# Kernel optimization log

Measured on AMD Instinct MI355X. Metric: run time of the kernel, lower is better.

## Reference

```python
import jax, jax.numpy as jnp
import numpy as np

NL, NK = 10000, 2000          # ligand / keypoint node counts
ELL, EKL = 320000, 160000     # lig->lig and kp->lig edge counts
IN, HID, OUT = 128, 128, 128  # in_size, hidden_size, out_size
FDIM = 2 * IN + 1             # edge MLP input: [h_src, h_dst, dij]


def silu(x):
    return x * jax.nn.sigmoid(x)


def setup_inputs() -> dict:
    keys = iter(jax.random.split(jax.random.key(0), 64))

    def nrm(shape, scale=0.02):
        return jax.random.normal(next(keys), shape, dtype=jnp.float32) * scale

    d = {}
    d["h_lig"] = jax.random.normal(next(keys), (NL, IN), dtype=jnp.float32)
    d["h_kp"] = jax.random.normal(next(keys), (NK, IN), dtype=jnp.float32)
    d["x_lig"] = jax.random.normal(next(keys), (NL, 3), dtype=jnp.float32)
    d["x_kp"] = jax.random.normal(next(keys), (NK, 3), dtype=jnp.float32)
    # per-node normalizer (e.g. neighbor count); keep >= 1 to avoid blowup
    d["z_lig"] = jax.random.uniform(next(keys), (NL, 1), dtype=jnp.float32, minval=1.0, maxval=32.0)
    for e in ("ll", "kl"):
        d[e + "_eW1"] = nrm((FDIM, HID)); d[e + "_eb1"] = jnp.zeros((HID,), jnp.float32)
        d[e + "_eW2"] = nrm((HID, HID)); d[e + "_eb2"] = jnp.zeros((HID,), jnp.float32)
        d[e + "_aW"] = nrm((HID, 1)); d[e + "_ab"] = jnp.zeros((1,), jnp.float32)
        d[e + "_cW1"] = nrm((FDIM, HID)); d[e + "_cb1"] = jnp.zeros((HID,), jnp.float32)
        d[e + "_cW2"] = nrm((HID, HID)); d[e + "_cb2"] = jnp.zeros((HID,), jnp.float32)
        d[e + "_cW3"] = nrm((HID, 1), scale=0.001)  # xavier gain=0.001 final coord layer
    d["n_W1"] = nrm((IN + HID, HID)); d["n_b1"] = jnp.zeros((HID,), jnp.float32)
    d["n_W2"] = nrm((HID, OUT)); d["n_b2"] = jnp.zeros((OUT,), jnp.float32)
    d["ll_src"] = jax.random.randint(next(keys), (ELL,), 0, NL, dtype=jnp.int32)
    d["ll_dst"] = jax.random.randint(next(keys), (ELL,), 0, NL, dtype=jnp.int32)
    d["kl_src"] = jax.random.randint(next(keys), (EKL,), 0, NK, dtype=jnp.int32)
    d["kl_dst"] = jax.random.randint(next(keys), (EKL,), 0, NL, dtype=jnp.int32)
    return d


def _edge_messages(hs, hd, xs, xd, eW1, eb1, eW2, eb2, aW, ab, cW1, cb1, cW2, cb2, cW3):
    x_diff = xs - xd                                     # fn.u_sub_v
    dij = jnp.linalg.norm(x_diff, axis=1, keepdims=True)  # [E,1]
    x_diff = x_diff / (dij + 1.0)
    f = jnp.concatenate([hs, hd, dij], axis=1)           # [E, 2*IN+1]
    m = silu(f @ eW1 + eb1)
    m = silu(m @ eW2 + eb2)
    msg_h = m * jax.nn.sigmoid(m @ aW + ab)              # soft attention gate
    c = silu(f @ cW1 + cb1)
    c = silu(c @ cW2 + cb2)
    msg_x = (c @ cW3) * x_diff                           # use_tanh=False path
    return msg_h, msg_x


def reference(h_lig, h_kp, x_lig, x_kp, z_lig,
              ll_eW1, ll_eb1, ll_eW2, ll_eb2, ll_aW, ll_ab,
              ll_cW1, ll_cb1, ll_cW2, ll_cb2, ll_cW3,
              kl_eW1, kl_eb1, kl_eW2, kl_eb2, kl_aW, kl_ab,
              kl_cW1, kl_cb1, kl_cW2, kl_cb2, kl_cW3,
              n_W1, n_b1, n_W2, n_b2,
              ll_src, ll_dst, kl_src, kl_dst):
    # lig -> lig edges
    mh_ll, mx_ll = _edge_messages(h_lig[ll_src], h_lig[ll_dst], x_lig[ll_src], x_lig[ll_dst],
                                  ll_eW1, ll_eb1, ll_eW2, ll_eb2, ll_aW, ll_ab,
                                  ll_cW1, ll_cb1, ll_cW2, ll_cb2, ll_cW3)
    # kp -> lig edges
    mh_kl, mx_kl = _edge_messages(h_kp[kl_src], h_lig[kl_dst], x_kp[kl_src], x_lig[kl_dst],
                                  kl_eW1, kl_eb1, kl_eW2, kl_eb2, kl_aW, kl_ab,
                                  kl_cW1, kl_cb1, kl_cW2, kl_cb2, kl_cW3)
    nl = h_lig.shape[0]
    # multi_update_all with cross_reducer='sum', then per-node normalization by z
    h_neigh = (jax.ops.segment_sum(mh_ll, ll_dst, num_segments=nl)
               + jax.ops.segment_sum(mh_kl, kl_dst, num_segments=nl)) / z_lig
    x_neigh = (jax.ops.segment_sum(mx_ll, ll_dst, num_segments=nl)
               + jax.ops.segment_sum(mx_kl, kl_dst, num_segments=nl)) / z_lig
    nin = jnp.concatenate([h_lig, h_neigh], axis=1)
    h_out = h_lig + (silu(nin @ n_W1 + n_b1) @ n_W2 + n_b2)  # norm=False -> Identity
    x_out = x_lig + x_neigh
    return (h_out, x_out)
```

## Files before the change

kernel.cpp:

```cpp
#include <hip/hip_runtime.h>
#include <math.h>

#define EPB  64
#define MSTR 136

typedef __attribute__((ext_vector_type(8))) short short8;
typedef __attribute__((ext_vector_type(4))) float f32x4;

__device__ __forceinline__ unsigned short f2bf(float x) {
    unsigned int u = __float_as_uint(x);
    u += 0x7fffu + ((u >> 16) & 1u);
    return (unsigned short)(u >> 16);
}
__device__ __forceinline__ float bf2f(short v) {
    return __uint_as_float(((unsigned int)(unsigned short)v) << 16);
}
__device__ __forceinline__ float fsilu(float x) {
    return x * (1.0f / (1.0f + __expf(-x)));
}
__device__ __forceinline__ float fsigm(float x) {
    return 1.0f / (1.0f + __expf(-x));
}
__device__ __forceinline__ void atomAddF(float* p, float v) {
    unsafeAtomicAdd(p, v);
}

struct PrepArgs { const float* src[10]; };

__global__ __launch_bounds__(256) void setup_kernel(PrepArgs pa, short* __restrict__ wsb,
                                                    float* __restrict__ out, int out_n,
                                                    int* __restrict__ hist) {
    int idx = blockIdx.x * 256 + threadIdx.x;
    if (idx < 245760) {
        int pair = idx / 49152;
        int rem  = idx - pair * 49152;
        int second = (rem >= 32768) ? 1 : 0;
        int mi = pair * 2 + second;
        int within = second ? (rem - 32768) : rem;
        int n, k, K;
        if (second) { K = 128; n = within >> 7; k = within & 127; }
        else        { K = 256; n = within >> 8; k = within & 255; }
        int dstoff = pair * 49152 + second * 32768;
        wsb[dstoff + n * K + k] = (short)f2bf(pa.src[mi][k * 128 + n]);
        return;
    }
    idx -= 245760;
    if (idx < out_n) { out[idx] = 0.0f; return; }
    idx -= out_n;
    if (idx < 20000) hist[idx] = 0;
}

__global__ __launch_bounds__(256) void hist_kernel(const int* __restrict__ lld,
                                                   const int* __restrict__ kld,
                                                   int* __restrict__ hist) {
    int i = blockIdx.x * 256 + threadIdx.x;
    if (i < 320000) atomicAdd(&hist[lld[i]], 1);
    else if (i < 480000) atomicAdd(&hist[10000 + kld[i - 320000]], 1);
}

__global__ __launch_bounds__(256) void scan_kernel(const int* __restrict__ hist,
                                                   int* __restrict__ cursor) {
    __shared__ int sbuf[256];
    const int b = blockIdx.x, t = threadIdx.x;
    const int* h = hist + b * 10000;
    int* cur = cursor + b * 10000;
    const int base = t * 40;
    int s = 0;
#pragma unroll 8
    for (int i = 0; i < 40; i++) if (base + i < 10000) s += h[base + i];
    sbuf[t] = s;
    __syncthreads();
    for (int off = 1; off < 256; off <<= 1) {
        int v = (t >= off) ? sbuf[t - off] : 0;
        __syncthreads();
        sbuf[t] += v;
        __syncthreads();
    }
    int run = sbuf[t] - s;
    for (int i = 0; i < 40; i++) {
        if (base + i < 10000) { cur[base + i] = run; run += h[base + i]; }
    }
}

__global__ __launch_bounds__(256) void scatter_kernel(const int* __restrict__ lls,
                                                      const int* __restrict__ lld,
                                                      const int* __restrict__ kls,
                                                      const int* __restrict__ kld,
                                                      int* __restrict__ cursor,
                                                      int* __restrict__ ll_ssrc, int* __restrict__ ll_sdst,
                                                      int* __restrict__ kl_ssrc, int* __restrict__ kl_sdst) {
    int i = blockIdx.x * 256 + threadIdx.x;
    if (i < 320000) {
        int d = lld[i];
        int p = atomicAdd(&cursor[d], 1);
        ll_ssrc[p] = lls[i]; ll_sdst[p] = d;
    } else if (i < 480000) {
        int j = i - 320000;
        int d = kld[j];
        int p = atomicAdd(&cursor[10000 + d], 1);
        kl_ssrc[p] = kls[j]; kl_sdst[p] = d;
    }
}

struct ProjDesc { const float* A; const short* Bt; short* out; const float* bias;
                  int rows; int ktb; int co; int hasb; };
struct ProjArgs { ProjDesc d[8]; };

__global__ __launch_bounds__(256) void proj_kernel(ProjArgs pa) {
    const ProjDesc pd = pa.d[blockIdx.y];
    const int tile = blockIdx.x;
    if (tile * 64 >= pd.rows) return;
    __shared__ __align__(16) short a_lds[64 * MSTR];
    const int t = threadIdx.x;
    {
        const int r = t >> 2, q = t & 3;
        const int node = tile * 64 + r;
        short* arow = a_lds + r * MSTR + q * 32;
        if (node < pd.rows) {
            const float* ap = pd.A + (size_t)node * 128 + q * 32;
#pragma unroll
            for (int i = 0; i < 4; i++) {
                float4 v0 = *(const float4*)(ap + i * 8);
                float4 v1 = *(const float4*)(ap + i * 8 + 4);
                short8 o;
                o[0] = (short)f2bf(v0.x); o[1] = (short)f2bf(v0.y);
                o[2] = (short)f2bf(v0.z); o[3] = (short)f2bf(v0.w);
                o[4] = (short)f2bf(v1.x); o[5] = (short)f2bf(v1.y);
                o[6] = (short)f2bf(v1.z); o[7] = (short)f2bf(v1.w);
                *(short8*)(arow + i * 8) = o;
            }
        } else {
            short8 z = {0, 0, 0, 0, 0, 0, 0, 0};
#pragma unroll
            for (int i = 0; i < 4; i++) *(short8*)(arow + i * 8) = z;
        }
    }
    __syncthreads();

    const int ln = t & 63, wv = t >> 6;
    const int lrow = ln & 15, quad = ln >> 4;
    const int c0 = wv * 32 + lrow, c1 = c0 + 16;

    short8 bf0[4], bf1[4];
#pragma unroll
    for (int kt = 0; kt < 4; kt++) {
        bf0[kt] = *(const short8*)(pd.Bt + c0 * 256 + (pd.ktb + kt) * 32 + quad * 8);
        bf1[kt] = *(const short8*)(pd.Bt + c1 * 256 + (pd.ktb + kt) * 32 + quad * 8);
    }
    const float bb0 = pd.hasb ? pd.bias[c0] : 0.0f;
    const float bb1 = pd.hasb ? pd.bias[c1] : 0.0f;
#pragma unroll
    for (int mt = 0; mt < 4; mt++) {
        short8 af[4];
#pragma unroll
        for (int kt = 0; kt < 4; kt++)
            af[kt] = *(const short8*)(&a_lds[(mt * 16 + lrow) * MSTR + kt * 32 + quad * 8]);
        f32x4 a0 = {0.f, 0.f, 0.f, 0.f}, a1 = {0.f, 0.f, 0.f, 0.f};
#pragma unroll
        for (int kt = 0; kt < 4; kt++) {
            a0 = __builtin_amdgcn_mfma_f32_16x16x32_bf16(af[kt], bf0[kt], a0, 0, 0, 0);
            a1 = __builtin_amdgcn_mfma_f32_16x16x32_bf16(af[kt], bf1[kt], a1, 0, 0, 0);
        }
#pragma unroll
        for (int r = 0; r < 4; r++) {
            const int node = tile * 64 + mt * 16 + quad * 4 + r;
            if (node < pd.rows) {
                pd.out[(size_t)node * 256 + pd.co + c0] = (short)f2bf(a0[r] + bb0);
                pd.out[(size_t)node * 256 + pd.co + c1] = (short)f2bf(a1[r] + bb1);
            }
        }
    }
}

struct EdgeSet {
    const short *Ps, *Pd;
    const float *xs, *xd;
    const int *esrc, *edst;
    const float *w256e, *w256c;
    const short *W2t, *cW2t;
    const float *b2e, *b2c;
    const float *aW, *ab, *cW3;
};
struct EdgePair { EdgeSet s[2]; int split; };

__global__ __launch_bounds__(256, 4) void edge_kernel(EdgePair ep,
                                                      float* __restrict__ hne,
                                                      float* __restrict__ xne)
{
    __shared__ __align__(16) char mbuf[34816];
    __shared__ float sv_l[EPB];
    __shared__ float gate_l[EPB];
    __shared__ float xdf[3][EPB];
    __shared__ int   dstl[EPB];
    __shared__ float gp[4][EPB];

    short* mh = (short*)mbuf;
    short* mc = (short*)(mbuf + 17408);
    float* msg = (float*)mbuf;

    const int isKL = (blockIdx.x >= ep.split) ? 1 : 0;
    const EdgeSet P = ep.s[isKL];
    const int bid = blockIdx.x - (isKL ? ep.split : 0);
    const int eb = bid * EPB;
    const int t = threadIdx.x;

    {
        const int e = t >> 2, q = t & 3;
        const int eid = eb + e;
        const int s = P.esrc[eid], d = P.edst[eid];
        float dx = P.xs[s * 3 + 0] - P.xd[d * 3 + 0];
        float dy = P.xs[s * 3 + 1] - P.xd[d * 3 + 1];
        float dz = P.xs[s * 3 + 2] - P.xd[d * 3 + 2];
        float dd = sqrtf(dx * dx + dy * dy + dz * dz);
        if (q == 0) {
            dstl[e] = d;
            float inv = 1.0f / (dd + 1.0f);
            xdf[0][e] = dx * inv; xdf[1][e] = dy * inv; xdf[2][e] = dz * inv;
        }
        const short* psrow = P.Ps + (size_t)s * 256 + q * 32;
        const short* pdrow = P.Pd + (size_t)d * 256 + q * 32;
#pragma unroll
        for (int path = 0; path < 2; path++) {
            const short* ps = psrow + path * 128;
            const short* pq = pdrow + path * 128;
            const float* wq = (path ? P.w256c : P.w256e) + q * 32;
            short* mrow = (path ? mc : mh) + e * MSTR + q * 32;
#pragma unroll
            for (int i = 0; i < 4; i++) {
                short8 a = *(const short8*)(ps + i * 8);
                short8 b = *(const short8*)(pq + i * 8);
                float4 wA = *(const float4*)(wq + i * 8);
                float4 wB = *(const float4*)(wq + i * 8 + 4);
                short8 o;
                o[0] = (short)f2bf(fsilu(bf2f(a[0]) + bf2f(b[0]) + dd * wA.x));
                o[1] = (short)f2bf(fsilu(bf2f(a[1]) + bf2f(b[1]) + dd * wA.y));
                o[2] = (short)f2bf(fsilu(bf2f(a[2]) + bf2f(b[2]) + dd * wA.z));
                o[3] = (short)f2bf(fsilu(bf2f(a[3]) + bf2f(b[3]) + dd * wA.w));
                o[4] = (short)f2bf(fsilu(bf2f(a[4]) + bf2f(b[4]) + dd * wB.x));
                o[5] = (short)f2bf(fsilu(bf2f(a[5]) + bf2f(b[5]) + dd * wB.y));
                o[6] = (short)f2bf(fsilu(bf2f(a[6]) + bf2f(b[6]) + dd * wB.z));
                o[7] = (short)f2bf(fsilu(bf2f(a[7]) + bf2f(b[7]) + dd * wB.w));
                *(short8*)(mrow + i * 8) = o;
            }
        }
    }
    __syncthreads();

    const int ln = t & 63, wv = t >> 6;
    const int lrow = ln & 15, quad = ln >> 4;
    const int c0 = wv * 32 + lrow, c1 = c0 + 16;

    {
        short8 bf0[4], bf1[4];
#pragma unroll
        for (int kt = 0; kt < 4; kt++) {
            bf0[kt] = *(const short8*)(P.cW2t + c0 * 128 + kt * 32 + quad * 8);
            bf1[kt] = *(const short8*)(P.cW2t + c1 * 128 + kt * 32 + quad * 8);
        }
        const float cw0 = P.cW3[c0], cw1 = P.cW3[c1];
        const float bb0 = P.b2c[c0], bb1 = P.b2c[c1];
#pragma unroll
        for (int mt = 0; mt < 4; mt++) {
            short8 af[4];
#pragma unroll
            for (int kt = 0; kt < 4; kt++)
                af[kt] = *(const short8*)(&mc[(mt * 16 + lrow) * MSTR + kt * 32 + quad * 8]);
            f32x4 a0 = {0.f, 0.f, 0.f, 0.f}, a1 = {0.f, 0.f, 0.f, 0.f};
#pragma unroll
            for (int kt = 0; kt < 4; kt++) {
                a0 = __builtin_amdgcn_mfma_f32_16x16x32_bf16(af[kt], bf0[kt], a0, 0, 0, 0);
                a1 = __builtin_amdgcn_mfma_f32_16x16x32_bf16(af[kt], bf1[kt], a1, 0, 0, 0);
            }
#pragma unroll
            for (int r = 0; r < 4; r++) {
                float v0 = fsilu(a0[r] + bb0);
                float v1 = fsilu(a1[r] + bb1);
                float g = v0 * cw0 + v1 * cw1;
                g += __shfl_xor(g, 1, 64);
                g += __shfl_xor(g, 2, 64);
                g += __shfl_xor(g, 4, 64);
                g += __shfl_xor(g, 8, 64);
                if (lrow == 0) gp[wv][mt * 16 + quad * 4 + r] = g;
            }
        }
    }
    __syncthreads();
    if (t < EPB) sv_l[t] = gp[0][t] + gp[1][t] + gp[2][t] + gp[3][t];
    __syncthreads();

    float m2s[4][8];
    {
        short8 bf0[4], bf1[4];
#pragma unroll
        for (int kt = 0; kt < 4; kt++) {
            bf0[kt] = *(const short8*)(P.W2t + c0 * 128 + kt * 32 + quad * 8);
            bf1[kt] = *(const short8*)(P.W2t + c1 * 128 + kt * 32 + quad * 8);
        }
        const float aw0 = P.aW[c0], aw1 = P.aW[c1];
        const float bb0 = P.b2e[c0], bb1 = P.b2e[c1];
#pragma unroll
        for (int mt = 0; mt < 4; mt++) {
            short8 af[4];
#pragma unroll
            for (int kt = 0; kt < 4; kt++)
                af[kt] = *(const short8*)(&mh[(mt * 16 + lrow) * MSTR + kt * 32 + quad * 8]);
            f32x4 a0 = {0.f, 0.f, 0.f, 0.f}, a1 = {0.f, 0.f, 0.f, 0.f};
#pragma unroll
            for (int kt = 0; kt < 4; kt++) {
                a0 = __builtin_amdgcn_mfma_f32_16x16x32_bf16(af[kt], bf0[kt], a0, 0, 0, 0);
                a1 = __builtin_amdgcn_mfma_f32_16x16x32_bf16(af[kt], bf1[kt], a1, 0, 0, 0);
            }
#pragma unroll
            for (int r = 0; r < 4; r++) {
                float v0 = fsilu(a0[r] + bb0);
                float v1 = fsilu(a1[r] + bb1);
                m2s[mt][r] = v0; m2s[mt][4 + r] = v1;
                float g = v0 * aw0 + v1 * aw1;
                g += __shfl_xor(g, 1, 64);
                g += __shfl_xor(g, 2, 64);
                g += __shfl_xor(g, 4, 64);
                g += __shfl_xor(g, 8, 64);
                if (lrow == 0) gp[wv][mt * 16 + quad * 4 + r] = g;
            }
        }
    }
    __syncthreads();
    if (t < EPB) gate_l[t] = fsigm(gp[0][t] + gp[1][t] + gp[2][t] + gp[3][t] + P.ab[0]);
    __syncthreads();

#pragma unroll
    for (int mt = 0; mt < 4; mt++)
#pragma unroll
        for (int r = 0; r < 4; r++) {
            const int erow = mt * 16 + quad * 4 + r;
            const float gv = gate_l[erow];
            msg[erow * 132 + c0] = m2s[mt][r] * gv;
            msg[erow * 132 + c1] = m2s[mt][4 + r] * gv;
        }
    __syncthreads();

    if (t < 128) {
        const int col = t;
        float acc = 0.0f;
        int cur = dstl[0];
#pragma unroll 4
        for (int e = 0; e < EPB; e++) {
            const int d = dstl[e];
            if (d != cur) {
                atomAddF(&hne[(size_t)cur * 128 + col], acc);
                acc = 0.0f; cur = d;
            }
            acc += msg[e * 132 + col];
        }
        atomAddF(&hne[(size_t)cur * 128 + col], acc);
    } else if (t < 131) {
        const int ax = t - 128;
        float acc = 0.0f;
        int cur = dstl[0];
        for (int e = 0; e < EPB; e++) {
            const int d = dstl[e];
            if (d != cur) {
                atomAddF(&xne[cur * 3 + ax], acc);
                acc = 0.0f; cur = d;
            }
            acc += sv_l[e] * xdf[ax][e];
        }
        atomAddF(&xne[cur * 3 + ax], acc);
    }
}

#define FSTR 264
__global__ __launch_bounds__(256) void node_kernel(
    const float* __restrict__ h_lig, const float* __restrict__ zlig,
    const short* __restrict__ W1t, const float* __restrict__ b1v,
    const short* __restrict__ W2t, const float* __restrict__ b2v,
    const float* __restrict__ x_lig,
    float* __restrict__ acc_h, float* __restrict__ acc_x)
{
    __shared__ __align__(16) short f_lds[64 * FSTR];
    __shared__ __align__(16) short m_lds[64 * MSTR];
    const int t = threadIdx.x;
    const int nb = blockIdx.x * 64;

    {
        const int e = t >> 2, q = t & 3;
        const int node = nb + e;
        short* frow = &f_lds[e * FSTR + q * 32];
        if (node < 10000) {
            const float zi = 1.0f / zlig[node];
            const float4* hp = (const float4*)(h_lig + (size_t)node * 128 + q * 32);
            const float4* np = (const float4*)(acc_h + (size_t)node * 128 + q * 32);
#pragma unroll
            for (int i = 0; i < 8; i++) {
                float4 v = hp[i];
                *(ushort4*)(frow + i * 4) =
                    make_ushort4(f2bf(v.x), f2bf(v.y), f2bf(v.z), f2bf(v.w));
            }
#pragma unroll
            for (int i = 0; i < 8; i++) {
                float4 v = np[i];
                *(ushort4*)(frow + 128 + i * 4) =
                    make_ushort4(f2bf(v.x * zi), f2bf(v.y * zi), f2bf(v.z * zi), f2bf(v.w * zi));
            }
        } else {
            const ushort4 zz = make_ushort4(0, 0, 0, 0);
#pragma unroll
            for (int i = 0; i < 8; i++) {
                *(ushort4*)(frow + i * 4) = zz;
                *(ushort4*)(frow + 128 + i * 4) = zz;
            }
        }
    }
    __syncthreads();

    const int ln = t & 63, wv = t >> 6;
    const int lrow = ln & 15, quad = ln >> 4;
    const int c0 = wv * 32 + lrow, c1 = c0 + 16;

    {
        short8 bf0[8], bf1[8];
#pragma unroll
        for (int kt = 0; kt < 8; kt++) {
            bf0[kt] = *(const short8*)(W1t + c0 * 256 + kt * 32 + quad * 8);
            bf1[kt] = *(const short8*)(W1t + c1 * 256 + kt * 32 + quad * 8);
        }
        const float bb0 = b1v[c0], bb1 = b1v[c1];
#pragma unroll
        for (int mt = 0; mt < 4; mt++) {
            short8 af[8];
#pragma unroll
            for (int kt = 0; kt < 8; kt++)
                af[kt] = *(const short8*)(&f_lds[(mt * 16 + lrow) * FSTR + kt * 32 + quad * 8]);
            f32x4 a0 = {0.f, 0.f, 0.f, 0.f}, a1 = {0.f, 0.f, 0.f, 0.f};
#pragma unroll
            for (int kt = 0; kt < 8; kt++) {
                a0 = __builtin_amdgcn_mfma_f32_16x16x32_bf16(af[kt], bf0[kt], a0, 0, 0, 0);
                a1 = __builtin_amdgcn_mfma_f32_16x16x32_bf16(af[kt], bf1[kt], a1, 0, 0, 0);
            }
#pragma unroll
            for (int r = 0; r < 4; r++) {
                const int erow = mt * 16 + quad * 4 + r;
                m_lds[erow * MSTR + c0] = (short)f2bf(fsilu(a0[r] + bb0));
                m_lds[erow * MSTR + c1] = (short)f2bf(fsilu(a1[r] + bb1));
            }
        }
    }
    __syncthreads();

    {
        short8 bf0[4], bf1[4];
#pragma unroll
        for (int kt = 0; kt < 4; kt++) {
            bf0[kt] = *(const short8*)(W2t + c0 * 128 + kt * 32 + quad * 8);
            bf1[kt] = *(const short8*)(W2t + c1 * 128 + kt * 32 + quad * 8);
        }
        const float bb0 = b2v[c0], bb1 = b2v[c1];
#pragma unroll
        for (int mt = 0; mt < 4; mt++) {
            short8 af[4];
#pragma unroll
            for (int kt = 0; kt < 4; kt++)
                af[kt] = *(const short8*)(&m_lds[(mt * 16 + lrow) * MSTR + kt * 32 + quad * 8]);
            f32x4 a0 = {0.f, 0.f, 0.f, 0.f}, a1 = {0.f, 0.f, 0.f, 0.f};
#pragma unroll
            for (int kt = 0; kt < 4; kt++) {
                a0 = __builtin_amdgcn_mfma_f32_16x16x32_bf16(af[kt], bf0[kt], a0, 0, 0, 0);
                a1 = __builtin_amdgcn_mfma_f32_16x16x32_bf16(af[kt], bf1[kt], a1, 0, 0, 0);
            }
#pragma unroll
            for (int r = 0; r < 4; r++) {
                const int node = nb + mt * 16 + quad * 4 + r;
                if (node < 10000) {
                    acc_h[(size_t)node * 128 + c0] = a0[r] + bb0 + h_lig[(size_t)node * 128 + c0];
                    acc_h[(size_t)node * 128 + c1] = a1[r] + bb1 + h_lig[(size_t)node * 128 + c1];
                }
            }
        }
    }
    if (t < 64) {
        const int node = nb + t;
        if (node < 10000) {
            const float zi = 1.0f / zlig[node];
#pragma unroll
            for (int i = 0; i < 3; i++)
                acc_x[node * 3 + i] = x_lig[node * 3 + i] + acc_x[node * 3 + i] * zi;
        }
    }
}

extern "C" void kernel_launch(void* const* d_in, const int* in_sizes, int n_in,
                              void* d_out, int out_size, void* d_ws, size_t ws_size,
                              hipStream_t stream)
{
    (void)in_sizes; (void)n_in; (void)ws_size;
    const float* h_lig  = (const float*)d_in[0];
    const float* h_kp   = (const float*)d_in[1];
    const float* x_lig  = (const float*)d_in[2];
    const float* x_kp   = (const float*)d_in[3];
    const float* z_lig  = (const float*)d_in[4];
    const float* ll_eW1 = (const float*)d_in[5];
    const float* ll_eb1 = (const float*)d_in[6];
    const float* ll_eW2 = (const float*)d_in[7];
    const float* ll_eb2 = (const float*)d_in[8];
    const float* ll_aW  = (const float*)d_in[9];
    const float* ll_ab  = (const float*)d_in[10];
    const float* ll_cW1 = (const float*)d_in[11];
    const float* ll_cb1 = (const float*)d_in[12];
    const float* ll_cW2 = (const float*)d_in[13];
    const float* ll_cb2 = (const float*)d_in[14];
    const float* ll_cW3 = (const float*)d_in[15];
    const float* kl_eW1 = (const float*)d_in[16];
    const float* kl_eb1 = (const float*)d_in[17];
    const float* kl_eW2 = (const float*)d_in[18];
    const float* kl_eb2 = (const float*)d_in[19];
    const float* kl_aW  = (const float*)d_in[20];
    const float* kl_ab  = (const float*)d_in[21];
    const float* kl_cW1 = (const float*)d_in[22];
    const float* kl_cb1 = (const float*)d_in[23];
    const float* kl_cW2 = (const float*)d_in[24];
    const float* kl_cb2 = (const float*)d_in[25];
    const float* kl_cW3 = (const float*)d_in[26];
    const float* n_W1   = (const float*)d_in[27];
    const float* n_b1   = (const float*)d_in[28];
    const float* n_W2   = (const float*)d_in[29];
    const float* n_b2   = (const float*)d_in[30];
    const int* ll_src = (const int*)d_in[31];
    const int* ll_dst = (const int*)d_in[32];
    const int* kl_src = (const int*)d_in[33];
    const int* kl_dst = (const int*)d_in[34];

    float* out = (float*)d_out;
    float* hne = out;
    float* xne = out + 1280000;

    char* wsc = (char*)d_ws;
    short* wsb    = (short*)wsc;
    short* P_ll_s = (short*)(wsc +   491520);
    short* P_ll_d = (short*)(wsc +  5611520);
    short* P_kl_s = (short*)(wsc + 10731520);
    short* P_kl_d = (short*)(wsc + 11755520);
    int* ll_ssrc  = (int*)(wsc + 16875520);
    int* ll_sdst  = (int*)(wsc + 18155520);
    int* kl_ssrc  = (int*)(wsc + 19435520);
    int* kl_sdst  = (int*)(wsc + 20075520);
    int* hist     = (int*)(wsc + 20715520);
    int* cursor   = (int*)(wsc + 20795520);

    {
        int total = 245760 + out_size + 20000;
        PrepArgs pa;
        pa.src[0] = ll_eW1; pa.src[1] = ll_eW2; pa.src[2] = ll_cW1; pa.src[3] = ll_cW2;
        pa.src[4] = kl_eW1; pa.src[5] = kl_eW2; pa.src[6] = kl_cW1; pa.src[7] = kl_cW2;
        pa.src[8] = n_W1;   pa.src[9] = n_W2;
        setup_kernel<<<(total + 255) / 256, 256, 0, stream>>>(pa, wsb, out, out_size, hist);
    }
    hist_kernel<<<1875, 256, 0, stream>>>(ll_dst, kl_dst, hist);
    scan_kernel<<<2, 256, 0, stream>>>(hist, cursor);
    scatter_kernel<<<1875, 256, 0, stream>>>(ll_src, ll_dst, kl_src, kl_dst, cursor,
                                             ll_ssrc, ll_sdst, kl_ssrc, kl_sdst);
    {
        ProjArgs pj;
        pj.d[0] = { h_lig, wsb + 0,      P_ll_s, ll_eb1, 10000, 0, 0,   0 };
        pj.d[1] = { h_lig, wsb + 49152,  P_ll_s, ll_cb1, 10000, 0, 128, 0 };
        pj.d[2] = { h_lig, wsb + 0,      P_ll_d, ll_eb1, 10000, 4, 0,   1 };
        pj.d[3] = { h_lig, wsb + 49152,  P_ll_d, ll_cb1, 10000, 4, 128, 1 };
        pj.d[4] = { h_kp,  wsb + 98304,  P_kl_s, kl_eb1,  2000, 0, 0,   0 };
        pj.d[5] = { h_kp,  wsb + 147456, P_kl_s, kl_cb1,  2000, 0, 128, 0 };
        pj.d[6] = { h_lig, wsb + 98304,  P_kl_d, kl_eb1, 10000, 4, 0,   1 };
        pj.d[7] = { h_lig, wsb + 147456, P_kl_d, kl_cb1, 10000, 4, 128, 1 };
        proj_kernel<<<dim3(157, 8), 256, 0, stream>>>(pj);
    }
    {
        EdgePair ep;
        ep.split = 5000;
        ep.s[0] = { P_ll_s, P_ll_d, x_lig, x_lig, ll_ssrc, ll_sdst,
                    ll_eW1 + 256 * 128, ll_cW1 + 256 * 128,
                    wsb + 32768, wsb + 81920, ll_eb2, ll_cb2,
                    ll_aW, ll_ab, ll_cW3 };
        ep.s[1] = { P_kl_s, P_kl_d, x_kp, x_lig, kl_ssrc, kl_sdst,
                    kl_eW1 + 256 * 128, kl_cW1 + 256 * 128,
                    wsb + 131072, wsb + 180224, kl_eb2, kl_cb2,
                    kl_aW, kl_ab, kl_cW3 };
        edge_kernel<<<7500, 256, 0, stream>>>(ep, hne, xne);
    }
    node_kernel<<<157, 256, 0, stream>>>(
        h_lig, z_lig, wsb + 196608, n_b1, wsb + 229376, n_b2,
        x_lig, hne, xne);
}
```

Baseline: 446.9 us.

## Fuse setup/hist and scatter/proj kernels, halve edge tile, raise occupancy

Merges the weight-conversion and histogram kernels into one launch and the scatter and projection kernels into another, and moves zeroing of the output and histogram to hipMemsetAsync. The scan now stages the histogram in LDS. The edge kernel processes 32 edges per block instead of 64, targets 8 blocks per CU, and applies the gate during the segmented reduction rather than in a separate pass with its own barrier. Together these cut launch count and aim to raise edge-kernel occupancy, at the cost of more blocks, more atomics per edge and less weight reuse per block.

```diff
diff --git a/kernel.cpp b/kernel.cpp
--- a/kernel.cpp
+++ b/kernel.cpp
@@ -1,8 +1,9 @@
 #include <hip/hip_runtime.h>
 #include <math.h>
 
-#define EPB  64
+#define EPB  32
 #define MSTR 136
+#define FSTR 264
 
 typedef __attribute__((ext_vector_type(8))) short short8;
 typedef __attribute__((ext_vector_type(4))) float f32x4;
@@ -27,9 +28,10 @@
 
 struct PrepArgs { const float* src[10]; };
 
-__global__ __launch_bounds__(256) void setup_kernel(PrepArgs pa, short* __restrict__ wsb,
-                                                    float* __restrict__ out, int out_n,
-                                                    int* __restrict__ hist) {
+__global__ __launch_bounds__(256) void prep_hist_kernel(PrepArgs pa, short* __restrict__ wsb,
+                                                        const int* __restrict__ lld,
+                                                        const int* __restrict__ kld,
+                                                        int* __restrict__ hist) {
     int idx = blockIdx.x * 256 + threadIdx.x;
     if (idx < 245760) {
         int pair = idx / 49152;
@@ -45,73 +47,71 @@
         return;
     }
     idx -= 245760;
-    if (idx < out_n) { out[idx] = 0.0f; return; }
-    idx -= out_n;
-    if (idx < 20000) hist[idx] = 0;
-}
-
-__global__ __launch_bounds__(256) void hist_kernel(const int* __restrict__ lld,
-                                                   const int* __restrict__ kld,
-                                                   int* __restrict__ hist) {
-    int i = blockIdx.x * 256 + threadIdx.x;
-    if (i < 320000) atomicAdd(&hist[lld[i]], 1);
-    else if (i < 480000) atomicAdd(&hist[10000 + kld[i - 320000]], 1);
+    if (idx < 320000) { atomicAdd(&hist[lld[idx]], 1); return; }
+    idx -= 320000;
+    if (idx < 160000) atomicAdd(&hist[10000 + kld[idx]], 1);
 }
 
 __global__ __launch_bounds__(256) void scan_kernel(const int* __restrict__ hist,
                                                    int* __restrict__ cursor) {
-    __shared__ int sbuf[256];
+    __shared__ int bins[10000];
+    __shared__ int ps[256];
     const int b = blockIdx.x, t = threadIdx.x;
     const int* h = hist + b * 10000;
     int* cur = cursor + b * 10000;
+    for (int i = t; i < 10000; i += 256) bins[i] = h[i];
+    __syncthreads();
     const int base = t * 40;
     int s = 0;
 #pragma unroll 8
-    for (int i = 0; i < 40; i++) if (base + i < 10000) s += h[base + i];
-    sbuf[t] = s;
+    for (int i = 0; i < 40; i++) { int ii = base + i; if (ii < 10000) s += bins[ii]; }
+    ps[t] = s;
     __syncthreads();
     for (int off = 1; off < 256; off <<= 1) {
-        int v = (t >= off) ? sbuf[t - off] : 0;
+        int v = (t >= off) ? ps[t - off] : 0;
         __syncthreads();
-        sbuf[t] += v;
+        ps[t] += v;
         __syncthreads();
     }
-    int run = sbuf[t] - s;
+    int run = ps[t] - s;
     for (int i = 0; i < 40; i++) {
-        if (base + i < 10000) { cur[base + i] = run; run += h[base + i]; }
-    }
-}
-
-__global__ __launch_bounds__(256) void scatter_kernel(const int* __restrict__ lls,
-                                                      const int* __restrict__ lld,
-                                                      const int* __restrict__ kls,
-                                                      const int* __restrict__ kld,
-                                                      int* __restrict__ cursor,
-                                                      int* __restrict__ ll_ssrc, int* __restrict__ ll_sdst,
-                                                      int* __restrict__ kl_ssrc, int* __restrict__ kl_sdst) {
-    int i = blockIdx.x * 256 + threadIdx.x;
-    if (i < 320000) {
-        int d = lld[i];
-        int p = atomicAdd(&cursor[d], 1);
-        ll_ssrc[p] = lls[i]; ll_sdst[p] = d;
-    } else if (i < 480000) {
-        int j = i - 320000;
-        int d = kld[j];
-        int p = atomicAdd(&cursor[10000 + d], 1);
-        kl_ssrc[p] = kls[j]; kl_sdst[p] = d;
-    }
+        int ii = base + i;
+        if (ii < 10000) { int c = bins[ii]; bins[ii] = run; run += c; }
+    }
+    __syncthreads();
+    for (int i = t; i < 10000; i += 256) cur[i] = bins[i];
 }
 
 struct ProjDesc { const float* A; const short* Bt; short* out; const float* bias;
                   int rows; int ktb; int co; int hasb; };
-struct ProjArgs { ProjDesc d[8]; };
-
-__global__ __launch_bounds__(256) void proj_kernel(ProjArgs pa) {
-    const ProjDesc pd = pa.d[blockIdx.y];
-    const int tile = blockIdx.x;
-    if (tile * 64 >= pd.rows) return;
+struct CArgs {
+    const int *lls, *lld, *kls, *kld;
+    int* cursor;
+    int *ll_ssrc, *ll_sdst, *kl_ssrc, *kl_sdst;
+    ProjDesc d[8];
+};
+
+__global__ __launch_bounds__(256) void scatter_proj_kernel(CArgs ca) {
     __shared__ __align__(16) short a_lds[64 * MSTR];
     const int t = threadIdx.x;
+    if (blockIdx.x < 1875) {
+        int i = blockIdx.x * 256 + t;
+        if (i < 320000) {
+            int d = ca.lld[i];
+            int p = atomicAdd(&ca.cursor[d], 1);
+            ca.ll_ssrc[p] = ca.lls[i]; ca.ll_sdst[p] = d;
+        } else if (i < 480000) {
+            int j = i - 320000;
+            int d = ca.kld[j];
+            int p = atomicAdd(&ca.cursor[10000 + d], 1);
+            ca.kl_ssrc[p] = ca.kls[j]; ca.kl_sdst[p] = d;
+        }
+        return;
+    }
+    const int pb = blockIdx.x - 1875;
+    const int di = pb / 157, tile = pb - di * 157;
+    const ProjDesc pd = ca.d[di];
+    if (tile * 64 >= pd.rows) return;
     {
         const int r = t >> 2, q = t & 3;
         const int node = tile * 64 + r;
@@ -183,11 +183,11 @@
 };
 struct EdgePair { EdgeSet s[2]; int split; };
 
-__global__ __launch_bounds__(256, 4) void edge_kernel(EdgePair ep,
+__global__ __launch_bounds__(256, 8) void edge_kernel(EdgePair ep,
                                                       float* __restrict__ hne,
                                                       float* __restrict__ xne)
 {
-    __shared__ __align__(16) char mbuf[34816];
+    __shared__ __align__(16) char mbuf[EPB * MSTR * 4];
     __shared__ float sv_l[EPB];
     __shared__ float gate_l[EPB];
     __shared__ float xdf[3][EPB];
@@ -195,17 +195,16 @@
     __shared__ float gp[4][EPB];
 
     short* mh = (short*)mbuf;
-    short* mc = (short*)(mbuf + 17408);
+    short* mc = (short*)(mbuf + EPB * MSTR * 2);
     float* msg = (float*)mbuf;
 
     const int isKL = (blockIdx.x >= ep.split) ? 1 : 0;
     const EdgeSet P = ep.s[isKL];
-    const int bid = blockIdx.x - (isKL ? ep.split : 0);
-    const int eb = bid * EPB;
+    const int eb = (blockIdx.x - (isKL ? ep.split : 0)) * EPB;
     const int t = threadIdx.x;
 
     {
-        const int e = t >> 2, q = t & 3;
+        const int e = t >> 3, q = t & 7;
         const int eid = eb + e;
         const int s = P.esrc[eid], d = P.edst[eid];
         float dx = P.xs[s * 3 + 0] - P.xd[d * 3 + 0];
@@ -217,16 +216,16 @@
             float inv = 1.0f / (dd + 1.0f);
             xdf[0][e] = dx * inv; xdf[1][e] = dy * inv; xdf[2][e] = dz * inv;
         }
-        const short* psrow = P.Ps + (size_t)s * 256 + q * 32;
-        const short* pdrow = P.Pd + (size_t)d * 256 + q * 32;
+        const short* psrow = P.Ps + (size_t)s * 256 + q * 16;
+        const short* pdrow = P.Pd + (size_t)d * 256 + q * 16;
 #pragma unroll
         for (int path = 0; path < 2; path++) {
             const short* ps = psrow + path * 128;
             const short* pq = pdrow + path * 128;
-            const float* wq = (path ? P.w256c : P.w256e) + q * 32;
-            short* mrow = (path ? mc : mh) + e * MSTR + q * 32;
-#pragma unroll
-            for (int i = 0; i < 4; i++) {
+            const float* wq = (path ? P.w256c : P.w256e) + q * 16;
+            short* mrow = (path ? mc : mh) + e * MSTR + q * 16;
+#pragma unroll
+            for (int i = 0; i < 2; i++) {
                 short8 a = *(const short8*)(ps + i * 8);
                 short8 b = *(const short8*)(pq + i * 8);
                 float4 wA = *(const float4*)(wq + i * 8);
@@ -260,7 +259,7 @@
         const float cw0 = P.cW3[c0], cw1 = P.cW3[c1];
         const float bb0 = P.b2c[c0], bb1 = P.b2c[c1];
 #pragma unroll
-        for (int mt = 0; mt < 4; mt++) {
+        for (int mt = 0; mt < 2; mt++) {
             short8 af[4];
 #pragma unroll
             for (int kt = 0; kt < 4; kt++)
@@ -288,7 +287,7 @@
     if (t < EPB) sv_l[t] = gp[0][t] + gp[1][t] + gp[2][t] + gp[3][t];
     __syncthreads();
 
-    float m2s[4][8];
+    float m2s[2][8];
     {
         short8 bf0[4], bf1[4];
 #pragma unroll
@@ -299,7 +298,7 @@
         const float aw0 = P.aW[c0], aw1 = P.aW[c1];
         const float bb0 = P.b2e[c0], bb1 = P.b2e[c1];
 #pragma unroll
-        for (int mt = 0; mt < 4; mt++) {
+        for (int mt = 0; mt < 2; mt++) {
             short8 af[4];
 #pragma unroll
             for (int kt = 0; kt < 4; kt++)
@@ -326,16 +325,13 @@
     }
     __syncthreads();
     if (t < EPB) gate_l[t] = fsigm(gp[0][t] + gp[1][t] + gp[2][t] + gp[3][t] + P.ab[0]);
-    __syncthreads();
-
-#pragma unroll
-    for (int mt = 0; mt < 4; mt++)
+#pragma unroll
+    for (int mt = 0; mt < 2; mt++)
 #pragma unroll
         for (int r = 0; r < 4; r++) {
             const int erow = mt * 16 + quad * 4 + r;
-            const float gv = gate_l[erow];
-            msg[erow * 132 + c0] = m2s[mt][r] * gv;
-            msg[erow * 132 + c1] = m2s[mt][4 + r] * gv;
+            msg[erow * 132 + c0] = m2s[mt][r];
+            msg[erow * 132 + c1] = m2s[mt][4 + r];
         }
     __syncthreads();
 
@@ -350,7 +346,7 @@
                 atomAddF(&hne[(size_t)cur * 128 + col], acc);
                 acc = 0.0f; cur = d;
             }
-            acc += msg[e * 132 + col];
+            acc += msg[e * 132 + col] * gate_l[e];
         }
         atomAddF(&hne[(size_t)cur * 128 + col], acc);
     } else if (t < 131) {
@@ -369,7 +365,6 @@
     }
 }
 
-#define FSTR 264
 __global__ __launch_bounds__(256) void node_kernel(
     const float* __restrict__ h_lig, const float* __restrict__ zlig,
     const short* __restrict__ W1t, const float* __restrict__ b1v,
@@ -546,33 +541,36 @@
     int* hist     = (int*)(wsc + 20715520);
     int* cursor   = (int*)(wsc + 20795520);
 
-    {
-        int total = 245760 + out_size + 20000;
+    hipMemsetAsync(d_out, 0, (size_t)out_size * sizeof(float), stream);
+    hipMemsetAsync(hist, 0, 80000, stream);
+
+    {
         PrepArgs pa;
         pa.src[0] = ll_eW1; pa.src[1] = ll_eW2; pa.src[2] = ll_cW1; pa.src[3] = ll_cW2;
         pa.src[4] = kl_eW1; pa.src[5] = kl_eW2; pa.src[6] = kl_cW1; pa.src[7] = kl_cW2;
         pa.src[8] = n_W1;   pa.src[9] = n_W2;
-        setup_kernel<<<(total + 255) / 256, 256, 0, stream>>>(pa, wsb, out, out_size, hist);
-    }
-    hist_kernel<<<1875, 256, 0, stream>>>(ll_dst, kl_dst, hist);
+        prep_hist_kernel<<<2835, 256, 0, stream>>>(pa, wsb, ll_dst, kl_dst, hist);
+    }
     scan_kernel<<<2, 256, 0, stream>>>(hist, cursor);
-    scatter_kernel<<<1875, 256, 0, stream>>>(ll_src, ll_dst, kl_src, kl_dst, cursor,
-                                             ll_ssrc, ll_sdst, kl_ssrc, kl_sdst);
-    {
-        ProjArgs pj;
-        pj.d[0] = { h_lig, wsb + 0,      P_ll_s, ll_eb1, 10000, 0, 0,   0 };
-        pj.d[1] = { h_lig, wsb + 49152,  P_ll_s, ll_cb1, 10000, 0, 128, 0 };
-        pj.d[2] = { h_lig, wsb + 0,      P_ll_d, ll_eb1, 10000, 4, 0,   1 };
-        pj.d[3] = { h_lig, wsb + 49152,  P_ll_d, ll_cb1, 10000, 4, 128, 1 };
-        pj.d[4] = { h_kp,  wsb + 98304,  P_kl_s, kl_eb1,  2000, 0, 0,   0 };
-        pj.d[5] = { h_kp,  wsb + 147456, P_kl_s, kl_cb1,  2000, 0, 128, 0 };
-        pj.d[6] = { h_lig, wsb + 98304,  P_kl_d, kl_eb1, 10000, 4, 0,   1 };
-        pj.d[7] = { h_lig, wsb + 147456, P_kl_d, kl_cb1, 10000, 4, 128, 1 };
-        proj_kernel<<<dim3(157, 8), 256, 0, stream>>>(pj);
+    {
+        CArgs ca;
+        ca.lls = ll_src; ca.lld = ll_dst; ca.kls = kl_src; ca.kld = kl_dst;
+        ca.cursor = cursor;
+        ca.ll_ssrc = ll_ssrc; ca.ll_sdst = ll_sdst;
+        ca.kl_ssrc = kl_ssrc; ca.kl_sdst = kl_sdst;
+        ca.d[0] = { h_lig, wsb + 0,      P_ll_s, ll_eb1, 10000, 0, 0,   0 };
+        ca.d[1] = { h_lig, wsb + 49152,  P_ll_s, ll_cb1, 10000, 0, 128, 0 };
+        ca.d[2] = { h_lig, wsb + 0,      P_ll_d, ll_eb1, 10000, 4, 0,   1 };
+        ca.d[3] = { h_lig, wsb + 49152,  P_ll_d, ll_cb1, 10000, 4, 128, 1 };
+        ca.d[4] = { h_kp,  wsb + 98304,  P_kl_s, kl_eb1,  2000, 0, 0,   0 };
+        ca.d[5] = { h_kp,  wsb + 147456, P_kl_s, kl_cb1,  2000, 0, 128, 0 };
+        ca.d[6] = { h_lig, wsb + 98304,  P_kl_d, kl_eb1, 10000, 4, 0,   1 };
+        ca.d[7] = { h_lig, wsb + 147456, P_kl_d, kl_cb1, 10000, 4, 128, 1 };
+        scatter_proj_kernel<<<1875 + 8 * 157, 256, 0, stream>>>(ca);
     }
     {
         EdgePair ep;
-        ep.split = 5000;
+        ep.split = 10000;
         ep.s[0] = { P_ll_s, P_ll_d, x_lig, x_lig, ll_ssrc, ll_sdst,
                     ll_eW1 + 256 * 128, ll_cW1 + 256 * 128,
                     wsb + 32768, wsb + 81920, ll_eb2, ll_cb2,
@@ -581,7 +579,7 @@
                     kl_eW1 + 256 * 128, kl_cW1 + 256 * 128,
                     wsb + 131072, wsb + 180224, kl_eb2, kl_cb2,
                     kl_aW, kl_ab, kl_cW3 };
-        edge_kernel<<<7500, 256, 0, stream>>>(ep, hne, xne);
+        edge_kernel<<<15000, 256, 0, stream>>>(ep, hne, xne);
     }
     node_kernel<<<157, 256, 0, stream>>>(
         h_lig, z_lig, wsb + 196608, n_b1, wsb + 229376, n_b2,
```

Result: faster. 412.5 us (-7.7%).
